# Kernel tuning notes

Measured on AMD Instinct MI355X. Metric: run time of the kernel, lower is better.

## Reference

```python
import jax, jax.numpy as jnp
import numpy as np

D_MODEL = 1024
N_HEADS = 16
HEAD_DIM = D_MODEL // N_HEADS
B, T = 4, 2048


def setup_inputs() -> dict:
    key = jax.random.key(0)
    ks = jax.random.split(key, 9)
    s = 1.0 / np.sqrt(D_MODEL)
    x = jax.random.normal(ks[0], (B, T, D_MODEL), dtype=jnp.float32)
    # causal mask: 1 = attend, 0 = blocked (masked_fill(mask == 0, -inf))
    mask = jnp.tril(jnp.ones((T, T), dtype=jnp.int32))[None, None, :, :]
    Wq = jax.random.uniform(ks[1], (D_MODEL, D_MODEL), jnp.float32, -s, s)
    bq = jax.random.uniform(ks[2], (D_MODEL,), jnp.float32, -s, s)
    Wk = jax.random.uniform(ks[3], (D_MODEL, D_MODEL), jnp.float32, -s, s)
    bk = jax.random.uniform(ks[4], (D_MODEL,), jnp.float32, -s, s)
    Wv = jax.random.uniform(ks[5], (D_MODEL, D_MODEL), jnp.float32, -s, s)
    bv = jax.random.uniform(ks[6], (D_MODEL,), jnp.float32, -s, s)
    Wo = jax.random.uniform(ks[7], (D_MODEL, D_MODEL), jnp.float32, -s, s)
    bo = jax.random.uniform(ks[8], (D_MODEL,), jnp.float32, -s, s)
    return {"x": x, "mask": mask, "Wq": Wq, "bq": bq, "Wk": Wk, "bk": bk,
            "Wv": Wv, "bv": bv, "Wo": Wo, "bo": bo}


def reference(x, mask, Wq, bq, Wk, bk, Wv, bv, Wo, bo):
    # nn.Linear: y = x @ W.T + b; here W stored as [in, out] so y = x @ W + b
    Bsz, Tlen, C = x.shape
    scale = jnp.sqrt(jnp.float32(HEAD_DIM))

    def split_heads(t):  # [B,T,C] -> [B,H,T,hd]
        return t.reshape(Bsz, Tlen, N_HEADS, HEAD_DIM).transpose(0, 2, 1, 3)

    Q = split_heads(x @ Wq + bq)
    K = split_heads(x @ Wk + bk)
    V = split_heads(x @ Wv + bv)

    scores = jnp.einsum("bhqd,bhkd->bhqk", Q, K) / scale
    scores = jnp.where(mask == 0, jnp.float32(-jnp.inf), scores)
    weights = jax.nn.softmax(scores, axis=-1)  # dropout is identity (eval/p=0)
    out = jnp.einsum("bhqk,bhkd->bhqd", weights, V)
    out = out.transpose(0, 2, 1, 3).reshape(Bsz, Tlen, C)
    return out @ Wo + bo
```

## Files before the change

### kernel.cpp

```cpp
#include <hip/hip_runtime.h>
#include <cstdint>
#include <cstddef>

#define B_SZ 4
#define T_SZ 2048
#define NH 16
#define HD 64
#define CD 1024
#define MROWS (B_SZ*T_SZ)
#define NEG_BIG (-1e30f)
#define Q_SCALE 0.180336880f

typedef __bf16 bf16x8 __attribute__((ext_vector_type(8)));
typedef __bf16 bf16x4 __attribute__((ext_vector_type(4)));
typedef short s16x4 __attribute__((ext_vector_type(4)));
typedef float f32x4 __attribute__((ext_vector_type(4)));

typedef __attribute__((address_space(3))) void* as3p;
typedef const __attribute__((address_space(1))) void* as1p;

__device__ __forceinline__ void glds16(const void* g, void* l) {
  __builtin_amdgcn_global_load_lds((as1p)g, (as3p)l, 16, 0, 0);
}

__global__ __launch_bounds__(256) void detect_dtype(const uint32_t* __restrict__ x,
                                                    int* __restrict__ flag) {
  __shared__ int cnt[256];
  const int t = threadIdx.x;
  int c = 0;
  for (int i = 0; i < 4; i++) {
    uint32_t w = x[t * 4 + i];
    uint32_t e = (w >> 7) & 0xFF;
    c += (e >= 100 && e <= 140) ? 1 : 0;
  }
  cnt[t] = c;
  __syncthreads();
  for (int s = 128; s > 0; s >>= 1) {
    if (t < s) cnt[t] += cnt[t + s];
    __syncthreads();
  }
  if (t == 0) flag[0] = (cnt[0] > 700) ? 1 : 0;
}

__device__ __forceinline__ bf16x8 cvt8(const void* src, int isbf, size_t i8) {
  bf16x8 o;
  if (isbf) {
    o = ((const bf16x8*)src)[i8];
  } else {
    const float4* s = (const float4*)((const float*)src + i8 * 8);
    float4 a = s[0], b = s[1];
    o[0] = (__bf16)a.x; o[1] = (__bf16)a.y; o[2] = (__bf16)a.z; o[3] = (__bf16)a.w;
    o[4] = (__bf16)b.x; o[5] = (__bf16)b.y; o[6] = (__bf16)b.z; o[7] = (__bf16)b.w;
  }
  return o;
}

__global__ __launch_bounds__(256) void conv_in(const void* __restrict__ src,
                                               const int* __restrict__ flag,
                                               __bf16* __restrict__ dst, int n8) {
  int i = blockIdx.x * 256 + threadIdx.x;
  if (i >= n8) return;
  ((bf16x8*)dst)[i] = cvt8(src, flag[0], i);
}

struct Ptr4 { const void* s[4]; __bf16* d[4]; };

__global__ __launch_bounds__(256) void conv_b4(Ptr4 p, const int* __restrict__ flag) {
  int i = threadIdx.x;
  if (i >= CD / 8) return;
  int which = blockIdx.x;
  ((bf16x8*)p.d[which])[i] = cvt8(p.s[which], flag[0], i);
}

__global__ __launch_bounds__(256) void transpose_conv4(Ptr4 p,
                                                       const int* __restrict__ flag) {
  __shared__ __align__(16) __bf16 tile[64 * 72];
  const void* W = p.s[blockIdx.z];
  __bf16* WT = p.d[blockIdx.z];
  const int t = threadIdx.x;
  const int r0 = blockIdx.y * 64, c0 = blockIdx.x * 64;
  const int rr = t >> 3, c8 = (t & 7) * 8;
  const int isbf = flag[0];
  for (int pp = 0; pp < 2; pp++) {
    int r = pp * 32 + rr;
    *(bf16x8*)(tile + r * 72 + c8) =
        cvt8(W, isbf, ((size_t)(r0 + r) * CD + c0 + c8) / 8);
  }
  __syncthreads();
  for (int pp = 0; pp < 2; pp++) {
    int cc = pp * 32 + rr;
    bf16x8 o;
    for (int j = 0; j < 8; j++) o[j] = tile[(c8 + j) * 72 + cc];
    *(bf16x8*)(WT + (size_t)(c0 + cc) * CD + r0 + c8) = o;
  }
}

__global__ __launch_bounds__(256) void gemm_qkv(
    const __bf16* __restrict__ A, const __bf16* __restrict__ BT,
    const __bf16* __restrict__ bias,
    __bf16* __restrict__ Qb, __bf16* __restrict__ Kb, __bf16* __restrict__ Vt) {
  __shared__ __align__(16) __bf16 As[128 * 64];
  __shared__ __align__(16) __bf16 Bs[128 * 64];
  const int tid = threadIdx.x;
  const int w = tid >> 6, lane = tid & 63;
  const int l15 = lane & 15, quad = lane >> 4;
  const int wm = w & 1, wn = w >> 1;
  const int bm = blockIdx.y, bn = blockIdx.x;
  const bool swapped = (bn < 16);

  f32x4 acc[4][4];
  for (int i = 0; i < 4; i++)
    for (int j = 0; j < 4; j++) acc[i][j] = (f32x4)0.f;

  const int srow = lane >> 3, scol = (lane & 7) * 8;
  const int scolsw = scol ^ (srow * 8);
  const __bf16* Abase = A + (size_t)(bm * 128) * CD;
  const __bf16* Bbase = BT + (size_t)(bn * 128) * CD;

  const int swz = (l15 & 7) * 8;
  for (int k0 = 0; k0 < CD; k0 += 64) {
    __syncthreads();
    for (int p = 0; p < 4; p++) {
      int seg = p * 4 + w;
      int row = seg * 8 + srow;
      glds16(Abase + (size_t)row * CD + k0 + scolsw, (char*)As + seg * 1024);
      glds16(Bbase + (size_t)row * CD + k0 + scolsw, (char*)Bs + seg * 1024);
    }
    __syncthreads();
    for (int kc = 0; kc < 2; kc++) {
      const int koff = (kc * 32 + quad * 8) ^ swz;
      bf16x8 af[4], bfr[4];
      for (int mt = 0; mt < 4; mt++)
        af[mt] = *(const bf16x8*)(As + (wm * 64 + mt * 16 + l15) * 64 + koff);
      for (int nt = 0; nt < 4; nt++)
        bfr[nt] = *(const bf16x8*)(Bs + (wn * 64 + nt * 16 + l15) * 64 + koff);
      if (swapped) {
        for (int mt = 0; mt < 4; mt++)
          for (int nt = 0; nt < 4; nt++)
            acc[mt][nt] = __builtin_amdgcn_mfma_f32_16x16x32_bf16(
                bfr[nt], af[mt], acc[mt][nt], 0, 0, 0);
      } else {
        for (int mt = 0; mt < 4; mt++)
          for (int nt = 0; nt < 4; nt++)
            acc[mt][nt] = __builtin_amdgcn_mfma_f32_16x16x32_bf16(
                af[mt], bfr[nt], acc[mt][nt], 0, 0, 0);
      }
    }
  }

  if (swapped) {
    const int hq = (bn & 7) * 2 + wn;
    const int bq_ = bm >> 4;
    const int tokb = (bm & 15) * 128 + wm * 64;
    __bf16* dst = (bn < 8) ? Qb : Kb;
    const float sc = (bn < 8) ? Q_SCALE : 1.f;
    for (int nt = 0; nt < 4; nt++) {
      const int d0 = nt * 16 + quad * 4;
      bf16x4 bv4 = *(const bf16x4*)(bias + bn * 128 + wn * 64 + d0);
      for (int mt = 0; mt < 4; mt++) {
        int tok = tokb + mt * 16 + l15;
        bf16x4 o;
        for (int r = 0; r < 4; r++)
          o[r] = (__bf16)((acc[mt][nt][r] + (float)bv4[r]) * sc);
        *(bf16x4*)(dst + ((size_t)(bq_ * NH + hq) * T_SZ + tok) * HD + d0) = o;
      }
    }
  } else {
    for (int nt = 0; nt < 4; nt++) {
      int col = bn * 128 + wn * 64 + nt * 16 + l15;
      int c = col & 1023, h = c >> 6, d = c & 63;
      float bv = (float)bias[col];
      for (int mt = 0; mt < 4; mt++) {
        int row0 = bm * 128 + wm * 64 + mt * 16 + quad * 4;
        int b = row0 >> 11, tok0 = row0 & 2047;
        bf16x4 o;
        for (int r = 0; r < 4; r++) o[r] = (__bf16)(acc[mt][nt][r] + bv);
        *(bf16x4*)(Vt + ((size_t)((b << 4) + h) * HD + d) * T_SZ + tok0) = o;
      }
    }
  }
}

__global__ __launch_bounds__(256) void gemm_out(
    const __bf16* __restrict__ A, const __bf16* __restrict__ BT,
    const __bf16* __restrict__ bias, void* __restrict__ Out,
    const int* __restrict__ flag) {
  __shared__ __align__(16) __bf16 As[128 * 64];
  __shared__ __align__(16) __bf16 Bs[128 * 64];
  const int tid = threadIdx.x;
  const int w = tid >> 6, lane = tid & 63;
  const int l15 = lane & 15, quad = lane >> 4;
  const int wm = w & 1, wn = w >> 1;
  const int bm = blockIdx.y, bn = blockIdx.x;

  f32x4 acc[4][4];
  for (int i = 0; i < 4; i++)
    for (int j = 0; j < 4; j++) acc[i][j] = (f32x4)0.f;

  const int srow = lane >> 3, scol = (lane & 7) * 8;
  const int scolsw = scol ^ (srow * 8);
  const __bf16* Abase = A + (size_t)(bm * 128) * CD;
  const __bf16* Bbase = BT + (size_t)(bn * 128) * CD;

  const int swz = (l15 & 7) * 8;
  for (int k0 = 0; k0 < CD; k0 += 64) {
    __syncthreads();
    for (int p = 0; p < 4; p++) {
      int seg = p * 4 + w;
      int row = seg * 8 + srow;
      glds16(Abase + (size_t)row * CD + k0 + scolsw, (char*)As + seg * 1024);
      glds16(Bbase + (size_t)row * CD + k0 + scolsw, (char*)Bs + seg * 1024);
    }
    __syncthreads();
    for (int kc = 0; kc < 2; kc++) {
      const int koff = (kc * 32 + quad * 8) ^ swz;
      bf16x8 af[4], bfr[4];
      for (int mt = 0; mt < 4; mt++)
        af[mt] = *(const bf16x8*)(As + (wm * 64 + mt * 16 + l15) * 64 + koff);
      for (int nt = 0; nt < 4; nt++)
        bfr[nt] = *(const bf16x8*)(Bs + (wn * 64 + nt * 16 + l15) * 64 + koff);
      for (int mt = 0; mt < 4; mt++)
        for (int nt = 0; nt < 4; nt++)
          acc[mt][nt] = __builtin_amdgcn_mfma_f32_16x16x32_bf16(
              bfr[nt], af[mt], acc[mt][nt], 0, 0, 0);
    }
  }

  const int isbf = flag[0];
  for (int nt = 0; nt < 4; nt++) {
    const int colb = bn * 128 + wn * 64 + nt * 16 + quad * 4;
    bf16x4 bv4 = *(const bf16x4*)(bias + colb);
    for (int mt = 0; mt < 4; mt++) {
      int row = bm * 128 + wm * 64 + mt * 16 + l15;
      if (isbf) {
        bf16x4 o;
        for (int r = 0; r < 4; r++)
          o[r] = (__bf16)(acc[mt][nt][r] + (float)bv4[r]);
        *(bf16x4*)((__bf16*)Out + (size_t)row * CD + colb) = o;
      } else {
        f32x4 o;
        for (int r = 0; r < 4; r++) o[r] = acc[mt][nt][r] + (float)bv4[r];
        *(f32x4*)((float*)Out + (size_t)row * CD + colb) = o;
      }
    }
  }
}

__global__ __launch_bounds__(512, 4) void attn(
    const __bf16* __restrict__ Q, const __bf16* __restrict__ K,
    const __bf16* __restrict__ Vt, __bf16* __restrict__ Y) {
  __shared__ __align__(16) __bf16 Ks[2][128 * 64];
  __shared__ __align__(16) __bf16 Vs[2][64 * 140];

  const int tid = threadIdx.x, w = tid >> 6, lane = tid & 63;
  const int l15 = lane & 15, quad = lane >> 4;
  const int lid = blockIdx.x + 8 * blockIdx.y;
  const int bh = lid & 63;
  const int pairi = lid >> 6;

  const __bf16* Qbh = Q + (size_t)bh * T_SZ * HD;
  const __bf16* Kbh = K + (size_t)bh * T_SZ * HD;
  const __bf16* Vbh = Vt + (size_t)bh * HD * T_SZ;

  const int srow = tid >> 3;
  const int scol = (tid & 7) * 8;
  const int ksrc = scol ^ ((srow & 7) * 8);
  const int b = bh >> 4, h = bh & 15;

  bf16x4 ones;
  for (int r = 0; r < 4; r++) ones[r] = (__bf16)1.0f;

  for (int ph = 0; ph < 2; ph++) {
    const int tq = ph ? (15 - pairi) : pairi;
    const int q0 = tq * 128;
    const int niter = tq + 1;
    const int qw = q0 + w * 16;

    __syncthreads();
    glds16(Kbh + (size_t)srow * HD + ksrc, (char*)Ks[0] + w * 1024);
    glds16(Kbh + (size_t)(64 + srow) * HD + ksrc,
           (char*)Ks[0] + 8192 + w * 1024);
    {
      bf16x8 va = *(const bf16x8*)(Vbh + (size_t)srow * T_SZ + scol);
      bf16x8 vb = *(const bf16x8*)(Vbh + (size_t)srow * T_SZ + 64 + scol);
      *(bf16x4*)(Vs[0] + srow * 140 + scol)          = ((bf16x4*)&va)[0];
      *(bf16x4*)(Vs[0] + srow * 140 + scol + 4)      = ((bf16x4*)&va)[1];
      *(bf16x4*)(Vs[0] + srow * 140 + 64 + scol)     = ((bf16x4*)&vb)[0];
      *(bf16x4*)(Vs[0] + srow * 140 + 64 + scol + 4) = ((bf16x4*)&vb)[1];
    }

    bf16x8 aq[2];
    for (int kc = 0; kc < 2; kc++)
      aq[kc] = *(const bf16x8*)(
          Qbh + (size_t)(qw + l15) * HD + kc * 32 + quad * 8);

    f32x4 acco[4];
    for (int dt = 0; dt < 4; dt++) acco[dt] = (f32x4)0.f;
    f32x4 accl = (f32x4)0.f;
    float m_ = NEG_BIG;

    for (int it = 0; it < niter; it++) {
      const int cur = it & 1;
      const int kv0 = it * 128;
      __syncthreads();

      bf16x8 vna, vnb;
      const bool havenext = (it + 1 < niter);
      if (havenext) {
        int kv1 = kv0 + 128;
        glds16(Kbh + (size_t)(kv1 + srow) * HD + ksrc,
               (char*)Ks[cur ^ 1] + w * 1024);
        glds16(Kbh + (size_t)(kv1 + 64 + srow) * HD + ksrc,
               (char*)Ks[cur ^ 1] + 8192 + w * 1024);
        vna = *(const bf16x8*)(Vbh + (size_t)srow * T_SZ + kv1 + scol);
        vnb = *(const bf16x8*)(Vbh + (size_t)srow * T_SZ + kv1 + 64 + scol);
      }

      if (kv0 <= qw + 15) {
        const __bf16* Ksc = Ks[cur];
        const __bf16* Vsc = Vs[cur];

        f32x4 accs[8];
        for (int nt = 0; nt < 8; nt++) accs[nt] = (f32x4)0.f;
        const int swz = (l15 & 7) * 8;
        for (int kc = 0; kc < 2; kc++)
          for (int nt = 0; nt < 8; nt++) {
            bf16x8 ak = *(const bf16x8*)(
                Ksc + (nt * 16 + l15) * 64 + ((kc * 32 + quad * 8) ^ swz));
            accs[nt] = __builtin_amdgcn_mfma_f32_16x16x32_bf16(
                ak, aq[kc], accs[nt], 0, 0, 0);
          }

        if (kv0 + 127 > qw) {
          int qg = qw + l15;
          for (int nt = 0; nt < 8; nt++) {
            int kg0 = kv0 + nt * 16 + quad * 4;
            for (int r = 0; r < 4; r++)
              if (kg0 + r > qg) accs[nt][r] = NEG_BIG;
          }
        }

        float tm[8];
        for (int nt = 0; nt < 8; nt++)
          tm[nt] = fmaxf(fmaxf(accs[nt][0], accs[nt][1]),
                         fmaxf(accs[nt][2], accs[nt][3]));
        float u0 = fmaxf(fmaxf(tm[0], tm[1]), fmaxf(tm[2], tm[3]));
        float u1 = fmaxf(fmaxf(tm[4], tm[5]), fmaxf(tm[6], tm[7]));
        float mloc = fmaxf(u0, u1);
        mloc = fmaxf(mloc, __shfl_xor(mloc, 16));
        mloc = fmaxf(mloc, __shfl_xor(mloc, 32));

        if (!__all(mloc <= m_)) {
          float mnew = fmaxf(m_, mloc);
          float alpha = __builtin_amdgcn_exp2f(m_ - mnew);
          m_ = mnew;
          accl[0] *= alpha;
          for (int dt = 0; dt < 4; dt++)
            for (int r = 0; r < 4; r++) acco[dt][r] *= alpha;
        }

        bf16x4 pf[8];
        for (int nt = 0; nt < 8; nt++)
          for (int r = 0; r < 4; r++)
            pf[nt][r] = (__bf16)__builtin_amdgcn_exp2f(accs[nt][r] - m_);

#pragma unroll
        for (int nt = 0; nt < 8; nt++) {
          accl = __builtin_amdgcn_mfma_f32_16x16x16bf16_1k(
              *(const s16x4*)&ones, *(const s16x4*)&pf[nt], accl, 0, 0, 0);
#pragma unroll
          for (int dt = 0; dt < 4; dt++) {
            bf16x4 av = *(const bf16x4*)(
                Vsc + (dt * 16 + l15) * 140 + nt * 16 + quad * 4);
            acco[dt] = __builtin_amdgcn_mfma_f32_16x16x16bf16_1k(
                *(const s16x4*)&av, *(const s16x4*)&pf[nt], acco[dt], 0, 0, 0);
          }
        }
      }

      if (havenext) {
        int nb = cur ^ 1;
        *(bf16x4*)(Vs[nb] + srow * 140 + scol)          = ((bf16x4*)&vna)[0];
        *(bf16x4*)(Vs[nb] + srow * 140 + scol + 4)      = ((bf16x4*)&vna)[1];
        *(bf16x4*)(Vs[nb] + srow * 140 + 64 + scol)     = ((bf16x4*)&vnb)[0];
        *(bf16x4*)(Vs[nb] + srow * 140 + 64 + scol + 4) = ((bf16x4*)&vnb)[1];
      }
    }

    {
      float rcp = 1.f / accl[0];
      int qg = qw + l15;
      size_t base = ((size_t)(b * T_SZ + qg)) * CD + h * HD + quad * 4;
      for (int dt = 0; dt < 4; dt++) {
        bf16x4 o;
        for (int r = 0; r < 4; r++) o[r] = (__bf16)(acco[dt][r] * rcp);
        *(bf16x4*)(Y + base + dt * 16) = o;
      }
    }
  }
}

extern "C" void kernel_launch(void* const* d_in, const int* in_sizes, int n_in,
                              void* d_out, int out_size, void* d_ws, size_t ws_size,
                              hipStream_t stream) {
  (void)in_sizes; (void)n_in; (void)out_size; (void)ws_size;
  const void* x  = d_in[0];
  const void* Wq = d_in[2];
  const void* bq = d_in[3];
  const void* Wk = d_in[4];
  const void* bk = d_in[5];
  const void* Wv = d_in[6];
  const void* bv = d_in[7];
  const void* Wo = d_in[8];
  const void* bo = d_in[9];

  char* ws = (char*)d_ws;
  const size_t MB = 1024 * 1024;
  __bf16* WqkvT = (__bf16*)(ws + 0 * MB);
  __bf16* WoT   = (__bf16*)(ws + 6 * MB);
  __bf16* bqkvc = (__bf16*)(ws + 8 * MB);
  __bf16* boc   = (__bf16*)(ws + 8 * MB + 8192);
  int*    flag  = (int*)   (ws + 8 * MB + 65536);
  __bf16* xc    = (__bf16*)(ws + 9 * MB);
  __bf16* Qb    = (__bf16*)(ws + 25 * MB);
  __bf16* Kb    = (__bf16*)(ws + 41 * MB);
  __bf16* Vt_g  = (__bf16*)(ws + 57 * MB);
  __bf16* Yb    = xc;

  dim3 tb(256);
  detect_dtype<<<1, tb, 0, stream>>>((const uint32_t*)x, flag);

  conv_in<<<4096, tb, 0, stream>>>(x, flag, xc, MROWS * CD / 8);
  Ptr4 pb = {{bq, bk, bv, bo}, {bqkvc, bqkvc + CD, bqkvc + 2 * CD, boc}};
  conv_b4<<<4, tb, 0, stream>>>(pb, flag);
  Ptr4 pw = {{Wq, Wk, Wv, Wo},
             {WqkvT, WqkvT + (size_t)CD * CD, WqkvT + 2 * (size_t)CD * CD, WoT}};
  transpose_conv4<<<dim3(16, 16, 4), tb, 0, stream>>>(pw, flag);

  gemm_qkv<<<dim3(24, MROWS / 128), tb, 0, stream>>>(xc, WqkvT, bqkvc, Qb, Kb, Vt_g);

  attn<<<dim3(8, B_SZ * NH), dim3(512), 0, stream>>>(Qb, Kb, Vt_g, Yb);

  gemm_out<<<dim3(CD / 128, MROWS / 128), tb, 0, stream>>>(Yb, WoT, boc, d_out, flag);
}
```

Baseline: 276.8 us.

## Double-buffer LDS tiles and remap workgroups for XCD locality in GEMMs

Both projection GEMMs (QKV and output) now use two LDS buffers per operand. Each iteration issues the asynchronous global-to-LDS load for the next K tile before computing on the current one, which is meant to hide global load latency behind MFMA work, and it cuts the barriers per iteration from two to one. The block index is also permuted so that consecutive blocks on the same XCD (round-robin by 8) work on neighbouring tiles, aiming for better L2 reuse. The cost is double the LDS footprint (64 KB per block), which may lower occupancy.

```diff
diff --git a/kernel.cpp b/kernel.cpp
--- a/kernel.cpp
+++ b/kernel.cpp
@@ -99,13 +99,15 @@
     const __bf16* __restrict__ A, const __bf16* __restrict__ BT,
     const __bf16* __restrict__ bias,
     __bf16* __restrict__ Qb, __bf16* __restrict__ Kb, __bf16* __restrict__ Vt) {
-  __shared__ __align__(16) __bf16 As[128 * 64];
-  __shared__ __align__(16) __bf16 Bs[128 * 64];
+  __shared__ __align__(16) __bf16 As[2][128 * 64];
+  __shared__ __align__(16) __bf16 Bs[2][128 * 64];
   const int tid = threadIdx.x;
   const int w = tid >> 6, lane = tid & 63;
   const int l15 = lane & 15, quad = lane >> 4;
   const int wm = w & 1, wn = w >> 1;
-  const int bm = blockIdx.y, bn = blockIdx.x;
+  const int orig = blockIdx.x + 24 * blockIdx.y;
+  const int wg = (orig & 7) * 192 + (orig >> 3);
+  const int bn = wg % 24, bm = wg / 24;
   const bool swapped = (bn < 16);
 
   f32x4 acc[4][4];
@@ -117,23 +119,28 @@
   const __bf16* Abase = A + (size_t)(bm * 128) * CD;
   const __bf16* Bbase = BT + (size_t)(bn * 128) * CD;
 
-  const int swz = (l15 & 7) * 8;
-  for (int k0 = 0; k0 < CD; k0 += 64) {
-    __syncthreads();
+  auto STAGE = [&](int buf, int k0) {
     for (int p = 0; p < 4; p++) {
       int seg = p * 4 + w;
       int row = seg * 8 + srow;
-      glds16(Abase + (size_t)row * CD + k0 + scolsw, (char*)As + seg * 1024);
-      glds16(Bbase + (size_t)row * CD + k0 + scolsw, (char*)Bs + seg * 1024);
-    }
+      glds16(Abase + (size_t)row * CD + k0 + scolsw, (char*)As[buf] + seg * 1024);
+      glds16(Bbase + (size_t)row * CD + k0 + scolsw, (char*)Bs[buf] + seg * 1024);
+    }
+  };
+
+  const int swz = (l15 & 7) * 8;
+  STAGE(0, 0);
+  for (int it = 0; it < 16; it++) {
+    const int cur = it & 1;
     __syncthreads();
+    if (it + 1 < 16) STAGE(cur ^ 1, (it + 1) * 64);
     for (int kc = 0; kc < 2; kc++) {
       const int koff = (kc * 32 + quad * 8) ^ swz;
       bf16x8 af[4], bfr[4];
       for (int mt = 0; mt < 4; mt++)
-        af[mt] = *(const bf16x8*)(As + (wm * 64 + mt * 16 + l15) * 64 + koff);
+        af[mt] = *(const bf16x8*)(As[cur] + (wm * 64 + mt * 16 + l15) * 64 + koff);
       for (int nt = 0; nt < 4; nt++)
-        bfr[nt] = *(const bf16x8*)(Bs + (wn * 64 + nt * 16 + l15) * 64 + koff);
+        bfr[nt] = *(const bf16x8*)(Bs[cur] + (wn * 64 + nt * 16 + l15) * 64 + koff);
       if (swapped) {
         for (int mt = 0; mt < 4; mt++)
           for (int nt = 0; nt < 4; nt++)
@@ -185,13 +192,15 @@
     const __bf16* __restrict__ A, const __bf16* __restrict__ BT,
     const __bf16* __restrict__ bias, void* __restrict__ Out,
     const int* __restrict__ flag) {
-  __shared__ __align__(16) __bf16 As[128 * 64];
-  __shared__ __align__(16) __bf16 Bs[128 * 64];
+  __shared__ __align__(16) __bf16 As[2][128 * 64];
+  __shared__ __align__(16) __bf16 Bs[2][128 * 64];
   const int tid = threadIdx.x;
   const int w = tid >> 6, lane = tid & 63;
   const int l15 = lane & 15, quad = lane >> 4;
   const int wm = w & 1, wn = w >> 1;
-  const int bm = blockIdx.y, bn = blockIdx.x;
+  const int orig = blockIdx.x + 8 * blockIdx.y;
+  const int wg = (orig & 7) * 64 + (orig >> 3);
+  const int bn = wg & 7, bm = wg >> 3;
 
   f32x4 acc[4][4];
   for (int i = 0; i < 4; i++)
@@ -202,23 +211,28 @@
   const __bf16* Abase = A + (size_t)(bm * 128) * CD;
   const __bf16* Bbase = BT + (size_t)(bn * 128) * CD;
 
-  const int swz = (l15 & 7) * 8;
-  for (int k0 = 0; k0 < CD; k0 += 64) {
-    __syncthreads();
+  auto STAGE = [&](int buf, int k0) {
     for (int p = 0; p < 4; p++) {
       int seg = p * 4 + w;
       int row = seg * 8 + srow;
-      glds16(Abase + (size_t)row * CD + k0 + scolsw, (char*)As + seg * 1024);
-      glds16(Bbase + (size_t)row * CD + k0 + scolsw, (char*)Bs + seg * 1024);
-    }
+      glds16(Abase + (size_t)row * CD + k0 + scolsw, (char*)As[buf] + seg * 1024);
+      glds16(Bbase + (size_t)row * CD + k0 + scolsw, (char*)Bs[buf] + seg * 1024);
+    }
+  };
+
+  const int swz = (l15 & 7) * 8;
+  STAGE(0, 0);
+  for (int it = 0; it < 16; it++) {
+    const int cur = it & 1;
     __syncthreads();
+    if (it + 1 < 16) STAGE(cur ^ 1, (it + 1) * 64);
     for (int kc = 0; kc < 2; kc++) {
       const int koff = (kc * 32 + quad * 8) ^ swz;
       bf16x8 af[4], bfr[4];
       for (int mt = 0; mt < 4; mt++)
-        af[mt] = *(const bf16x8*)(As + (wm * 64 + mt * 16 + l15) * 64 + koff);
+        af[mt] = *(const bf16x8*)(As[cur] + (wm * 64 + mt * 16 + l15) * 64 + koff);
       for (int nt = 0; nt < 4; nt++)
-        bfr[nt] = *(const bf16x8*)(Bs + (wn * 64 + nt * 16 + l15) * 64 + koff);
+        bfr[nt] = *(const bf16x8*)(Bs[cur] + (wn * 64 + nt * 16 + l15) * 64 + koff);
       for (int mt = 0; mt < 4; mt++)
         for (int nt = 0; nt < 4; nt++)
           acc[mt][nt] = __builtin_amdgcn_mfma_f32_16x16x32_bf16(
```

Measured after the change: 283.0 us. 1.02x slower.
